# Optimization experiments

Measured on AMD Instinct MI355X. Metric: run time of the kernel, lower is better.

Reference implementation:

```python
import jax, jax.numpy as jnp
import numpy as np

N_QUBITS = 10
DEPTH = 4


def _cz_sign(n):
    # Diagonal of product of CZ(q, q+1) for q in 0..n-2 (qubit q = bit q, little-endian).
    idx = np.arange(2 ** n)
    bits = (idx[:, None] >> np.arange(n)) & 1            # (2^n, n)
    pairs = (bits[:, :-1] & bits[:, 1:]).sum(axis=1)
    return jnp.asarray(1 - 2 * (pairs & 1), jnp.float32)  # (2^n,)


def _z_matrix(n):
    # Column i = diagonal of Z on qubit n-1-i (Qiskit label 'I'*i + 'Z' + ...).
    idx = np.arange(2 ** n)
    bits = (idx[:, None] >> np.arange(n)) & 1
    return jnp.asarray((1 - 2 * bits)[:, ::-1], jnp.float32)  # (2^n, n)


def _quantum_features(x, theta):
    B, n = x.shape
    depth = theta.shape[0]
    half = 0.5 * x
    c = jnp.cos(half).astype(jnp.complex64)
    s = jnp.sin(half).astype(jnp.complex64)
    # Initial state: per-sample product of RX(x_q)|0> = [cos(x/2), -i sin(x/2)].
    # Build as kron over qubits, MSB (qubit n-1) first -> flat index bit q = qubit q.
    state = jnp.ones((B, 1), jnp.complex64)
    for q in reversed(range(n)):
        v = jnp.stack([c[:, q], -1j * s[:, q]], axis=-1)  # (B, 2)
        state = (state[:, :, None] * v[:, None, :]).reshape(B, -1)
    cz = _cz_sign(n)
    for l in range(depth):
        for q in range(n):
            th = 0.5 * theta[l, q]
            ct = jnp.cos(th).astype(jnp.complex64)
            st = jnp.sin(th).astype(jnp.complex64)
            gate = jnp.stack([jnp.stack([ct, -st]), jnp.stack([st, ct])])  # (2,2) RY
            left, right = 2 ** (n - 1 - q), 2 ** q
            state = jnp.einsum('ij,bljr->blir', gate,
                               state.reshape(B, left, 2, right)).reshape(B, -1)
        state = state * cz  # all CZ(q,q+1) at once (diagonal)
    probs = state.real ** 2 + state.imag ** 2          # (B, 2^n)
    return probs @ _z_matrix(n)                        # (B, n) <Z_i> expectations


def setup_inputs() -> dict:
    key = jax.random.key(0)
    ks = jax.random.split(key, 6)
    B, F, D = 4096, N_QUBITS, DEPTH
    x = jax.random.normal(ks[0], (B, F), jnp.float32)
    Ws = jax.random.normal(ks[1], (D + 1, F, F), jnp.float32) / np.sqrt(F).astype(np.float32)
    bs = 0.01 * jax.random.normal(ks[2], (D + 1, F), jnp.float32)
    theta = jax.random.normal(ks[3], (D, F), jnp.float32)
    W_final = jax.random.normal(ks[4], (2, 2 * F), jnp.float32) / np.sqrt(2 * F).astype(np.float32)
    b_final = 0.01 * jax.random.normal(ks[5], (2,), jnp.float32)
    return {"x": x, "Ws": Ws, "bs": bs, "theta": theta,
            "W_final": W_final, "b_final": b_final}


def reference(x, Ws, bs, theta, W_final, b_final):
    # Classical stack: depth x (Linear + ReLU) then a final Linear (same width).
    h = x
    for l in range(DEPTH):
        h = jax.nn.relu(h @ Ws[l].T + bs[l])
    cls_out = h @ Ws[DEPTH].T + bs[DEPTH]              # (B, F)
    qfeat = _quantum_features(x, theta)                # (B, n_qubits)
    combined = jnp.concatenate([cls_out, qfeat], axis=1)
    return combined @ W_final.T + b_final              # (B, 2) logits
```

## Files before the change

kernel.cpp:

```cpp
#include <hip/hip_runtime.h>
#include <math.h>

#define NQ 10
#define QDEPTH 4
#define BLK 256
#define WPS 4

typedef float v2f __attribute__((ext_vector_type(2)));

__device__ __forceinline__ int   asi(float v) { return __builtin_bit_cast(int, v); }
__device__ __forceinline__ float asf(int v)   { return __builtin_bit_cast(float, v); }

__device__ __forceinline__ v2f pk_mul(v2f a, v2f b) {
    v2f d; asm("v_pk_mul_f32 %0, %1, %2" : "=v"(d) : "v"(a), "v"(b)); return d;
}
__device__ __forceinline__ v2f pk_fma(v2f a, v2f b, v2f c) {
    v2f d; asm("v_pk_fma_f32 %0, %1, %2, %3" : "=v"(d) : "v"(a), "v"(b), "v"(c)); return d;
}

template<int D>
__device__ __forceinline__ float exch(float v, int addr32) {
    if constexpr (D == 1)
        return asf(__builtin_amdgcn_update_dpp(asi(v), asi(v), 0xB1, 0xF, 0xF, true));
    else if constexpr (D == 2)
        return asf(__builtin_amdgcn_update_dpp(asi(v), asi(v), 0x4E, 0xF, 0xF, true));
    else if constexpr (D == 4)
        return asf(__builtin_amdgcn_ds_swizzle(asi(v), 0x101F));
    else if constexpr (D == 8)
        return asf(__builtin_amdgcn_ds_swizzle(asi(v), 0x201F));
    else if constexpr (D == 16)
        return asf(__builtin_amdgcn_ds_swizzle(asi(v), 0x401F));
    else
        return asf(__builtin_amdgcn_ds_bpermute(addr32, asi(v)));
}

__device__ __forceinline__ float rlane(float v, int l) {
    return asf(__builtin_amdgcn_readlane(asi(v), l));
}

template<int Q>
__device__ __forceinline__ void local_gate(v2f (&P)[16], float ct, float st) {
    v2f ct2 = {ct, ct}, st2 = {st, st}, nst2 = {-st, -st};
    #pragma unroll
    for (int pp = 0; pp < 8; ++pp) {
        const int i0 = ((pp >> Q) << (Q + 1)) | (pp & ((1 << Q) - 1));
        const int i1 = i0 | (1 << Q);
        v2f a = P[i0], b = P[i1];
        P[i0] = pk_fma(nst2, b, pk_mul(ct2, a));
        P[i1] = pk_fma(st2,  a, pk_mul(ct2, b));
    }
}

template<int D>
__device__ __forceinline__ void cross_gate(v2f (&P)[16], float ct, float stv, int addr32) {
    v2f ct2 = {ct, ct}, sv2 = {stv, stv};
    #pragma unroll
    for (int r = 0; r < 16; ++r) {
        v2f pp;
        pp.x = exch<D>(P[r].x, addr32);
        pp.y = exch<D>(P[r].y, addr32);
        P[r] = pk_fma(sv2, pp, pk_mul(ct2, P[r]));
    }
}

__global__ __launch_bounds__(BLK, 4) void hybrid_kernel(
    const float* __restrict__ x,
    const float* __restrict__ Ws,
    const float* __restrict__ bs,
    const float* __restrict__ theta,
    const float* __restrict__ Wf,
    const float* __restrict__ bfin,
    float* __restrict__ out)
{
    const int tid  = threadIdx.x;
    const int lane = tid & 63;
    const int wv   = tid >> 6;
    const int s    = blockIdx.x * WPS + wv;

    float ang = 0.0f;
    if (lane < QDEPTH * NQ)              ang = theta[lane];
    else if (lane < QDEPTH * NQ + NQ)    ang = x[s * NQ + (lane - QDEPTH * NQ)];
    float sv_, cv_;
    sincosf(0.5f * ang, &sv_, &cv_);

    float cq[NQ], sq[NQ];
    #pragma unroll
    for (int q = 0; q < NQ; ++q) {
        cq[q] = rlane(cv_, QDEPTH * NQ + q);
        sq[q] = rlane(sv_, QDEPTH * NQ + q);
    }
    float lf = 1.0f;
    #pragma unroll
    for (int b = 0; b < 6; ++b)
        lf *= ((lane >> b) & 1) ? sq[4 + b] : cq[4 + b];

    const int pl = __popc(lane);
    v2f P[16];
    {
        float p01[4], p23[4];
        p01[0] = cq[0] * cq[1]; p01[1] = sq[0] * cq[1];
        p01[2] = cq[0] * sq[1]; p01[3] = sq[0] * sq[1];
        p23[0] = cq[2] * cq[3]; p23[1] = sq[2] * cq[3];
        p23[2] = cq[2] * sq[3]; p23[3] = sq[2] * sq[3];
        #pragma unroll
        for (int loc = 0; loc < 16; ++loc) {
            float r = lf * p01[loc & 3] * p23[loc >> 2];
            int pm = (pl + __popc(loc)) & 3;
            P[loc].x = (pm == 0) ? r : ((pm == 2) ? -r : 0.0f);
            P[loc].y = (pm == 1) ? -r : ((pm == 3) ? r : 0.0f);
        }
    }

    int zmask[6];
    #pragma unroll
    for (int b = 0; b < 6; ++b)
        zmask[b] = ((lane >> b) & 1) << 31;
    const int addr32 = (lane ^ 32) << 2;

    const int p3  = __popc(lane & (lane >> 1)) & 1;
    const int sAw = p3 << 31;
    const int sBw = (p3 ^ (lane & 1)) << 31;
    const int sAn = sAw ^ 0x80000000;
    const int sBn = sBw ^ 0x80000000;

    for (int l = 0; l < QDEPTH; ++l) {
        local_gate<0>(P, rlane(cv_, l * NQ + 0), rlane(sv_, l * NQ + 0));
        local_gate<1>(P, rlane(cv_, l * NQ + 1), rlane(sv_, l * NQ + 1));
        local_gate<2>(P, rlane(cv_, l * NQ + 2), rlane(sv_, l * NQ + 2));
        local_gate<3>(P, rlane(cv_, l * NQ + 3), rlane(sv_, l * NQ + 3));
        {
            float ct, stv;
            ct  = rlane(cv_, l * NQ + 4);
            stv = asf(asi(-rlane(sv_, l * NQ + 4)) ^ zmask[0]);
            cross_gate<1>(P, ct, stv, addr32);
            ct  = rlane(cv_, l * NQ + 5);
            stv = asf(asi(-rlane(sv_, l * NQ + 5)) ^ zmask[1]);
            cross_gate<2>(P, ct, stv, addr32);
            ct  = rlane(cv_, l * NQ + 6);
            stv = asf(asi(-rlane(sv_, l * NQ + 6)) ^ zmask[2]);
            cross_gate<4>(P, ct, stv, addr32);
            ct  = rlane(cv_, l * NQ + 7);
            stv = asf(asi(-rlane(sv_, l * NQ + 7)) ^ zmask[3]);
            cross_gate<8>(P, ct, stv, addr32);
            ct  = rlane(cv_, l * NQ + 8);
            stv = asf(asi(-rlane(sv_, l * NQ + 8)) ^ zmask[4]);
            cross_gate<16>(P, ct, stv, addr32);
            ct  = rlane(cv_, l * NQ + 9);
            stv = asf(asi(-rlane(sv_, l * NQ + 9)) ^ zmask[5]);
            cross_gate<32>(P, ct, stv, addr32);
        }
        #pragma unroll
        for (int loc = 0; loc < 16; ++loc) {
            const int C1 = __popc(loc & (loc >> 1)) & 1;
            const int m  = (loc & 8) ? (C1 ? sBn : sBw) : (C1 ? sAn : sAw);
            P[loc].x = asf(asi(P[loc].x) ^ m);
            P[loc].y = asf(asi(P[loc].y) ^ m);
        }
    }

    float pr[16], S = 0.0f;
    #pragma unroll
    for (int loc = 0; loc < 16; ++loc) {
        v2f Q = pk_mul(P[loc], P[loc]);
        pr[loc] = Q.x + Q.y;
        S += pr[loc];
    }
    float U0 = 0.0f, U1 = 0.0f, U2 = 0.0f, U3 = 0.0f;
    #pragma unroll
    for (int loc = 0; loc < 16; ++loc) {
        if (loc & 1) U0 += pr[loc];
        if (loc & 2) U1 += pr[loc];
        if (loc & 4) U2 += pr[loc];
        if (loc & 8) U3 += pr[loc];
    }
    const float w00 = Wf[19], w01 = Wf[18], w02 = Wf[17], w03 = Wf[16];
    const float w10 = Wf[39], w11 = Wf[38], w12 = Wf[37], w13 = Wf[36];
    float d0 = ((w00 + w01) + (w02 + w03)) * S;
    float d1 = ((w10 + w11) + (w12 + w13)) * S;
    d0 = fmaf(-2.0f * w00, U0, d0); d0 = fmaf(-2.0f * w01, U1, d0);
    d0 = fmaf(-2.0f * w02, U2, d0); d0 = fmaf(-2.0f * w03, U3, d0);
    d1 = fmaf(-2.0f * w10, U0, d1); d1 = fmaf(-2.0f * w11, U1, d1);
    d1 = fmaf(-2.0f * w12, U2, d1); d1 = fmaf(-2.0f * w13, U3, d1);
    float L0 = 0.0f, L1 = 0.0f;
    #pragma unroll
    for (int b = 0; b < 6; ++b) {
        L0 += asf(asi(Wf[15 - b]) ^ zmask[b]);
        L1 += asf(asi(Wf[35 - b]) ^ zmask[b]);
    }
    float qp0 = fmaf(L0, S, d0);
    float qp1 = fmaf(L1, S, d1);
    qp0 += exch<1>(qp0, addr32);  qp1 += exch<1>(qp1, addr32);
    qp0 += exch<2>(qp0, addr32);  qp1 += exch<2>(qp1, addr32);
    qp0 += exch<4>(qp0, addr32);  qp1 += exch<4>(qp1, addr32);
    qp0 += exch<8>(qp0, addr32);  qp1 += exch<8>(qp1, addr32);
    qp0 += exch<16>(qp0, addr32); qp1 += exch<16>(qp1, addr32);
    qp0 += exch<32>(qp0, addr32); qp1 += exch<32>(qp1, addr32);

    const int row = (lane < NQ) ? lane : 0;
    float h = x[s * NQ + row];
    #pragma unroll
    for (int l = 0; l < QDEPTH; ++l) {
        float v = bs[l * NQ + row];
        #pragma unroll
        for (int j = 0; j < NQ; ++j)
            v = fmaf(Ws[(l * NQ + row) * NQ + j], rlane(h, j), v);
        h = fmaxf(v, 0.0f);
    }
    float cls = bs[QDEPTH * NQ + row];
    #pragma unroll
    for (int j = 0; j < NQ; ++j)
        cls = fmaf(Ws[(QDEPTH * NQ + row) * NQ + j], rlane(h, j), cls);

    float o0 = bfin[0] + qp0, o1 = bfin[1] + qp1;
    #pragma unroll
    for (int j = 0; j < NQ; ++j) {
        float cj = rlane(cls, j);
        o0 = fmaf(Wf[j],      cj, o0);
        o1 = fmaf(Wf[20 + j], cj, o1);
    }
    if (lane == 0) {
        float2 o; o.x = o0; o.y = o1;
        *reinterpret_cast<float2*>(&out[s * 2]) = o;
    }
}

extern "C" void kernel_launch(void* const* d_in, const int* in_sizes, int n_in,
                              void* d_out, int out_size, void* d_ws, size_t ws_size,
                              hipStream_t stream) {
    const float* x     = (const float*)d_in[0];
    const float* Ws    = (const float*)d_in[1];
    const float* bs    = (const float*)d_in[2];
    const float* theta = (const float*)d_in[3];
    const float* Wf    = (const float*)d_in[4];
    const float* bfin  = (const float*)d_in[5];
    float* out = (float*)d_out;

    const int B = in_sizes[0] / NQ;
    hybrid_kernel<<<B / WPS, BLK, 0, stream>>>(x, Ws, bs, theta, Wf, bfin, out);
}
```

Before: 26.95 us.

## Factor cosines out of RY gates, apply tangent-only gates and rescale probabilities

Each RY gate is rewritten as cos times [[1,-tan],[tan,1]], so every gate update needs one FMA per element instead of a multiply plus an FMA. The product of all rotation cosines is computed once with a lane reduction, squared, and applied to the final expectation contribution. This halves the floating-point work in the state-vector loop but brings numerical risk when a cosine is near zero, where the tangent becomes very large. The inline-asm packed ops are replaced with vector expressions left to the compiler.

```diff
diff --git a/kernel.cpp b/kernel.cpp
--- a/kernel.cpp
+++ b/kernel.cpp
@@ -10,13 +10,6 @@
 
 __device__ __forceinline__ int   asi(float v) { return __builtin_bit_cast(int, v); }
 __device__ __forceinline__ float asf(int v)   { return __builtin_bit_cast(float, v); }
-
-__device__ __forceinline__ v2f pk_mul(v2f a, v2f b) {
-    v2f d; asm("v_pk_mul_f32 %0, %1, %2" : "=v"(d) : "v"(a), "v"(b)); return d;
-}
-__device__ __forceinline__ v2f pk_fma(v2f a, v2f b, v2f c) {
-    v2f d; asm("v_pk_fma_f32 %0, %1, %2, %3" : "=v"(d) : "v"(a), "v"(b), "v"(c)); return d;
-}
 
 template<int D>
 __device__ __forceinline__ float exch(float v, int addr32) {
@@ -39,27 +32,27 @@
 }
 
 template<int Q>
-__device__ __forceinline__ void local_gate(v2f (&P)[16], float ct, float st) {
-    v2f ct2 = {ct, ct}, st2 = {st, st}, nst2 = {-st, -st};
+__device__ __forceinline__ void local_gate_t(v2f (&P)[16], float t) {
+    const v2f tt = {t, t};
     #pragma unroll
     for (int pp = 0; pp < 8; ++pp) {
         const int i0 = ((pp >> Q) << (Q + 1)) | (pp & ((1 << Q) - 1));
         const int i1 = i0 | (1 << Q);
         v2f a = P[i0], b = P[i1];
-        P[i0] = pk_fma(nst2, b, pk_mul(ct2, a));
-        P[i1] = pk_fma(st2,  a, pk_mul(ct2, b));
+        P[i0] = a - tt * b;
+        P[i1] = b + tt * a;
     }
 }
 
 template<int D>
-__device__ __forceinline__ void cross_gate(v2f (&P)[16], float ct, float stv, int addr32) {
-    v2f ct2 = {ct, ct}, sv2 = {stv, stv};
+__device__ __forceinline__ void cross_gate_t(v2f (&P)[16], float tvv, int addr32) {
+    const v2f tt = {tvv, tvv};
     #pragma unroll
     for (int r = 0; r < 16; ++r) {
         v2f pp;
         pp.x = exch<D>(P[r].x, addr32);
         pp.y = exch<D>(P[r].y, addr32);
-        P[r] = pk_fma(sv2, pp, pk_mul(ct2, P[r]));
+        P[r] = P[r] + tt * pp;
     }
 }
 
@@ -82,21 +75,35 @@
     else if (lane < QDEPTH * NQ + NQ)    ang = x[s * NQ + (lane - QDEPTH * NQ)];
     float sv_, cv_;
     sincosf(0.5f * ang, &sv_, &cv_);
-
-    float cq[NQ], sq[NQ];
-    #pragma unroll
-    for (int q = 0; q < NQ; ++q) {
-        cq[q] = rlane(cv_, QDEPTH * NQ + q);
-        sq[q] = rlane(sv_, QDEPTH * NQ + q);
-    }
-    float lf = 1.0f;
-    #pragma unroll
-    for (int b = 0; b < 6; ++b)
-        lf *= ((lane >> b) & 1) ? sq[4 + b] : cq[4 + b];
+    const float tv_ = sv_ / cv_;
+
+    const int addr32 = (lane ^ 32) << 2;
+
+    float cc = (lane < QDEPTH * NQ) ? cv_ : 1.0f;
+    cc *= exch<1>(cc, addr32);
+    cc *= exch<2>(cc, addr32);
+    cc *= exch<4>(cc, addr32);
+    cc *= exch<8>(cc, addr32);
+    cc *= exch<16>(cc, addr32);
+    cc *= exch<32>(cc, addr32);
+    const float C2 = cc * cc;
 
     const int pl = __popc(lane);
     v2f P[16];
     {
+        float cq[4], sq[4];
+        #pragma unroll
+        for (int q = 0; q < 4; ++q) {
+            cq[q] = rlane(cv_, QDEPTH * NQ + q);
+            sq[q] = rlane(sv_, QDEPTH * NQ + q);
+        }
+        float lf = 1.0f;
+        #pragma unroll
+        for (int b = 0; b < 6; ++b) {
+            float cb = rlane(cv_, QDEPTH * NQ + 4 + b);
+            float sb = rlane(sv_, QDEPTH * NQ + 4 + b);
+            lf *= ((lane >> b) & 1) ? sb : cb;
+        }
         float p01[4], p23[4];
         p01[0] = cq[0] * cq[1]; p01[1] = sq[0] * cq[1];
         p01[2] = cq[0] * sq[1]; p01[3] = sq[0] * sq[1];
@@ -115,7 +122,6 @@
     #pragma unroll
     for (int b = 0; b < 6; ++b)
         zmask[b] = ((lane >> b) & 1) << 31;
-    const int addr32 = (lane ^ 32) << 2;
 
     const int p3  = __popc(lane & (lane >> 1)) & 1;
     const int sAw = p3 << 31;
@@ -124,30 +130,24 @@
     const int sBn = sBw ^ 0x80000000;
 
     for (int l = 0; l < QDEPTH; ++l) {
-        local_gate<0>(P, rlane(cv_, l * NQ + 0), rlane(sv_, l * NQ + 0));
-        local_gate<1>(P, rlane(cv_, l * NQ + 1), rlane(sv_, l * NQ + 1));
-        local_gate<2>(P, rlane(cv_, l * NQ + 2), rlane(sv_, l * NQ + 2));
-        local_gate<3>(P, rlane(cv_, l * NQ + 3), rlane(sv_, l * NQ + 3));
+        local_gate_t<0>(P, rlane(tv_, l * NQ + 0));
+        local_gate_t<1>(P, rlane(tv_, l * NQ + 1));
+        local_gate_t<2>(P, rlane(tv_, l * NQ + 2));
+        local_gate_t<3>(P, rlane(tv_, l * NQ + 3));
         {
-            float ct, stv;
-            ct  = rlane(cv_, l * NQ + 4);
-            stv = asf(asi(-rlane(sv_, l * NQ + 4)) ^ zmask[0]);
-            cross_gate<1>(P, ct, stv, addr32);
-            ct  = rlane(cv_, l * NQ + 5);
-            stv = asf(asi(-rlane(sv_, l * NQ + 5)) ^ zmask[1]);
-            cross_gate<2>(P, ct, stv, addr32);
-            ct  = rlane(cv_, l * NQ + 6);
-            stv = asf(asi(-rlane(sv_, l * NQ + 6)) ^ zmask[2]);
-            cross_gate<4>(P, ct, stv, addr32);
-            ct  = rlane(cv_, l * NQ + 7);
-            stv = asf(asi(-rlane(sv_, l * NQ + 7)) ^ zmask[3]);
-            cross_gate<8>(P, ct, stv, addr32);
-            ct  = rlane(cv_, l * NQ + 8);
-            stv = asf(asi(-rlane(sv_, l * NQ + 8)) ^ zmask[4]);
-            cross_gate<16>(P, ct, stv, addr32);
-            ct  = rlane(cv_, l * NQ + 9);
-            stv = asf(asi(-rlane(sv_, l * NQ + 9)) ^ zmask[5]);
-            cross_gate<32>(P, ct, stv, addr32);
+            float tvv;
+            tvv = asf(asi(-rlane(tv_, l * NQ + 4)) ^ zmask[0]);
+            cross_gate_t<1>(P, tvv, addr32);
+            tvv = asf(asi(-rlane(tv_, l * NQ + 5)) ^ zmask[1]);
+            cross_gate_t<2>(P, tvv, addr32);
+            tvv = asf(asi(-rlane(tv_, l * NQ + 6)) ^ zmask[2]);
+            cross_gate_t<4>(P, tvv, addr32);
+            tvv = asf(asi(-rlane(tv_, l * NQ + 7)) ^ zmask[3]);
+            cross_gate_t<8>(P, tvv, addr32);
+            tvv = asf(asi(-rlane(tv_, l * NQ + 8)) ^ zmask[4]);
+            cross_gate_t<16>(P, tvv, addr32);
+            tvv = asf(asi(-rlane(tv_, l * NQ + 9)) ^ zmask[5]);
+            cross_gate_t<32>(P, tvv, addr32);
         }
         #pragma unroll
         for (int loc = 0; loc < 16; ++loc) {
@@ -161,8 +161,7 @@
     float pr[16], S = 0.0f;
     #pragma unroll
     for (int loc = 0; loc < 16; ++loc) {
-        v2f Q = pk_mul(P[loc], P[loc]);
-        pr[loc] = Q.x + Q.y;
+        pr[loc] = fmaf(P[loc].x, P[loc].x, P[loc].y * P[loc].y);
         S += pr[loc];
     }
     float U0 = 0.0f, U1 = 0.0f, U2 = 0.0f, U3 = 0.0f;
@@ -211,7 +210,8 @@
     for (int j = 0; j < NQ; ++j)
         cls = fmaf(Ws[(QDEPTH * NQ + row) * NQ + j], rlane(h, j), cls);
 
-    float o0 = bfin[0] + qp0, o1 = bfin[1] + qp1;
+    float o0 = fmaf(C2, qp0, bfin[0]);
+    float o1 = fmaf(C2, qp1, bfin[1]);
     #pragma unroll
     for (int j = 0; j < NQ; ++j) {
         float cj = rlane(cls, j);
```

Result: faster. 24.79 us (-8.0%).
